# Kernel tuning notes

Hardware: AMD Instinct MI355X
Metric: run time of the kernel (lower is better)

## Reference

```python
import jax, jax.numpy as jnp
import numpy as np
import math

B, S, DIN, DQ, DV = 8, 2048, 1024, 1024, 1024


def setup_inputs() -> dict:
    key = jax.random.key(0)
    ks = jax.random.split(key, 9)
    c_q = math.sqrt(6.0 / (DIN + DQ))
    c_v = math.sqrt(6.0 / (DIN + DV))
    query = jax.random.normal(ks[0], (B, S, DIN), dtype=jnp.float32)
    key_t = jax.random.normal(ks[1], (B, S, DIN), dtype=jnp.float32)
    value = jax.random.normal(ks[2], (B, S, DIN), dtype=jnp.float32)
    # Linear weights stored as [in, out] for x @ W; uniform init per module
    Wq = jax.random.uniform(ks[3], (DIN, DQ), jnp.float32, -c_q, c_q)
    Wk = jax.random.uniform(ks[4], (DIN, DQ), jnp.float32, -c_q, c_q)
    Wv = jax.random.uniform(ks[5], (DIN, DV), jnp.float32, -c_v, c_v)
    bq = jax.random.uniform(ks[6], (DQ,), jnp.float32, -c_q, c_q)
    bk = jax.random.uniform(ks[7], (DQ,), jnp.float32, -c_q, c_q)
    bv = jax.random.uniform(ks[8], (DV,), jnp.float32, -c_v, c_v)
    # causal mask: True where attention is disallowed (masked_fill semantics)
    mask = jnp.broadcast_to(jnp.triu(jnp.ones((S, S), dtype=bool), k=1), (B, S, S))
    return {"query": query, "key": key_t, "value": value,
            "Wq": Wq, "bq": bq, "Wk": Wk, "bk": bk, "Wv": Wv, "bv": bv,
            "mask": mask}


def reference(query, key, value, Wq, bq, Wk, bk, Wv, bv, mask):
    q = query @ Wq + bq                       # [B,S,DQ]
    k = key @ Wk + bk                         # [B,S,DQ]
    v = value @ Wv + bv                       # [B,S,DV]
    scores = jnp.einsum('bsd,btd->bst', q, k) / math.sqrt(DQ)  # [B,S,S]
    scores = jnp.where(mask, jnp.float32(-1e9), scores)
    weights = jax.nn.softmax(scores, axis=2)
    y = jnp.einsum('bst,btd->bsd', weights, v)  # [B,S,DV]
    return y
```

## Files before the change

kernel.cpp:

```cpp
#include <hip/hip_runtime.h>


typedef unsigned short u16;
typedef unsigned int   u32;
typedef float f32x4 __attribute__((ext_vector_type(4)));
typedef short s16x8 __attribute__((ext_vector_type(8)));

__device__ __forceinline__ u16 f2bf(float x) {
  u32 u = __builtin_bit_cast(u32, x);
  u += 0x7fffu + ((u >> 16) & 1u);
  return (u16)(u >> 16);
}
__device__ __forceinline__ float bf2f(u16 h) {
  u32 u = (u32)h << 16;
  return __builtin_bit_cast(float, u);
}

__device__ __forceinline__ void gld_lds16(const u16* g, u16* l) {
  __builtin_amdgcn_global_load_lds((const __attribute__((address_space(1))) void*)g,
                                   (__attribute__((address_space(3))) void*)l,
                                   16, 0, 0);
}

__global__ __launch_bounds__(256) void cvt_bf16_3(const float* __restrict__ i0,
                                                  const float* __restrict__ i1,
                                                  const float* __restrict__ i2,
                                                  u16* __restrict__ out, long X) {
  const float* in = blockIdx.y == 0 ? i0 : (blockIdx.y == 1 ? i1 : i2);
  long i = (long)blockIdx.x * 256 + threadIdx.x;
  float4 v = ((const float4*)in)[i];
  ushort4 o;
  o.x = f2bf(v.x); o.y = f2bf(v.y); o.z = f2bf(v.z); o.w = f2bf(v.w);
  ((ushort4*)(out + blockIdx.y * X))[i] = o;
}

__global__ __launch_bounds__(256) void transpose_w3(const float* __restrict__ w0,
                                                    const float* __restrict__ w1,
                                                    const float* __restrict__ w2,
                                                    u16* __restrict__ Wt,
                                                    int K, int N, long WN) {
  __shared__ u16 t[32][33];
  const float* W = blockIdx.z == 0 ? w0 : (blockIdx.z == 1 ? w1 : w2);
  u16* out = Wt + blockIdx.z * WN;
  int n0 = blockIdx.x * 32, k0 = blockIdx.y * 32;
  int tx = threadIdx.x & 31, ty = threadIdx.x >> 5;
  for (int r = ty; r < 32; r += 8)
    t[r][tx] = f2bf(W[(long)(k0 + r) * N + n0 + tx]);
  __syncthreads();
  for (int r = ty; r < 32; r += 8)
    out[(long)(n0 + r) * K + k0 + tx] = t[tx][r];
}

__global__ __launch_bounds__(256) void transpose_v(const u16* __restrict__ v,
                                                   u16* __restrict__ vt,
                                                   int S, int D) {
  __shared__ u16 t[32][33];
  long b = blockIdx.z;
  const u16* vb = v + b * S * D;
  u16* vtb = vt + b * S * D;
  int d0 = blockIdx.x * 32, s0 = blockIdx.y * 32;
  int tx = threadIdx.x & 31, ty = threadIdx.x >> 5;
  for (int r = ty; r < 32; r += 8)
    t[r][tx] = vb[(long)(s0 + r) * D + d0 + tx];
  __syncthreads();
  for (int r = ty; r < 32; r += 8)
    vtb[(long)(d0 + r) * S + s0 + tx] = t[tx][r];
}

__device__ __forceinline__ void gemm_core(const u16* __restrict__ At,
                                          const u16* __restrict__ Bt,
                                          int lda, int ldb, int ktEnd,
                                          f32x4 (&acc)[4][4],
                                          u16* lA, u16* lB) {
  const int tid = threadIdx.x;
  const int lane = tid & 63, half = lane >> 4, l16 = lane & 15;
  const int wave = tid >> 6;
  const int wm = (wave >> 1) * 64, wn = (wave & 1) * 64;

  const int c0 = tid, c1 = tid + 256;
  const int r0 = c0 >> 2, kp0 = (c0 & 3) ^ ((c0 >> 3) & 3);
  const int r1 = c1 >> 2, kp1 = (c1 & 3) ^ ((c1 >> 3) & 3);
  const u16* gA0 = At + (long)r0 * lda + kp0 * 8;
  const u16* gA1 = At + (long)r1 * lda + kp1 * 8;
  const u16* gB0 = Bt + (long)r0 * ldb + kp0 * 8;
  const u16* gB1 = Bt + (long)r1 * ldb + kp1 * 8;
  u16* lA0 = lA + c0 * 8; u16* lA1 = lA + c1 * 8;
  u16* lB0 = lB + c0 * 8; u16* lB1 = lB + c1 * 8;
  const int swz = (half ^ ((l16 >> 1) & 3)) * 8;

  for (int kt = 0; kt < ktEnd; ++kt) {
    const int k0 = kt * 32;
    gld_lds16(gA0 + k0, lA0);
    gld_lds16(gA1 + k0, lA1);
    gld_lds16(gB0 + k0, lB0);
    gld_lds16(gB1 + k0, lB1);
    __syncthreads();
    s16x8 af[4], bfr[4];
#pragma unroll
    for (int mi = 0; mi < 4; ++mi)
      af[mi] = *(const s16x8*)&lA[(wm + mi * 16 + l16) * 32 + swz];
#pragma unroll
    for (int ni = 0; ni < 4; ++ni)
      bfr[ni] = *(const s16x8*)&lB[(wn + ni * 16 + l16) * 32 + swz];
#pragma unroll
    for (int mi = 0; mi < 4; ++mi)
#pragma unroll
      for (int ni = 0; ni < 4; ++ni)
        acc[mi][ni] = __builtin_amdgcn_mfma_f32_16x16x32_bf16(af[mi], bfr[ni], acc[mi][ni], 0, 0, 0);
    __syncthreads();
  }
}

struct ProjPtrs {
  const u16* A[3];
  const u16* B[3];
  u16* C[3];
  const float* bias[3];
};

__global__ __launch_bounds__(256, 2)
void gemm_proj(ProjPtrs p, int lda, int ldb, int ldc, int kTiles) {
  const int f = blockIdx.x;
  const int xcd = f & 7;
  const int g = f >> 3;
  const int bz = g >> 7;
  const int l = g & 127;
  const int bm = (xcd << 4) + (l >> 3);
  const int bn = l & 7;

  __shared__ u16 lA[128 * 32], lB[128 * 32];
  f32x4 acc[4][4];
#pragma unroll
  for (int i = 0; i < 4; ++i)
#pragma unroll
    for (int j = 0; j < 4; ++j) { f32x4 z = {0.f, 0.f, 0.f, 0.f}; acc[i][j] = z; }

  gemm_core(p.A[bz] + (long)bm * 128 * lda, p.B[bz] + (long)bn * 128 * ldb,
            lda, ldb, kTiles, acc, lA, lB);

  const int lane = threadIdx.x & 63, half = lane >> 4, l16 = lane & 15;
  const int wave = threadIdx.x >> 6;
  const int wm = (wave >> 1) * 64, wn = (wave & 1) * 64;
  const int colBase = bn * 128 + wn + l16;
  const int rowBase = bm * 128 + wm + half * 4;
  u16* Cb = p.C[bz];
  const float* bias = p.bias[bz];
#pragma unroll
  for (int mi = 0; mi < 4; ++mi)
#pragma unroll
    for (int ni = 0; ni < 4; ++ni) {
      int col = colBase + ni * 16;
      float bv = bias[col];
#pragma unroll
      for (int r = 0; r < 4; ++r)
        Cb[(long)(rowBase + mi * 16 + r) * ldc + col] = f2bf(acc[mi][ni][r] + bv);
    }
}

__global__ __launch_bounds__(256, 2)
void gemm_scores_exp(const u16* __restrict__ q, const u16* __restrict__ k,
                     u16* __restrict__ E, int ld, long sQK, long sSC,
                     int kTiles, float scale) {
  const int f = blockIdx.x;
  const int bz = f & 7;
  const int t = f >> 3;
  int bm = (int)((sqrtf(8.f * t + 1.f) - 1.f) * 0.5f);
  while ((bm + 1) * (bm + 2) / 2 <= t) ++bm;
  while (bm * (bm + 1) / 2 > t) --bm;
  const int bn = t - bm * (bm + 1) / 2;

  __shared__ u16 lA[128 * 32], lB[128 * 32];
  f32x4 acc[4][4];
#pragma unroll
  for (int i = 0; i < 4; ++i)
#pragma unroll
    for (int j = 0; j < 4; ++j) { f32x4 z = {0.f, 0.f, 0.f, 0.f}; acc[i][j] = z; }

  gemm_core(q + (long)bz * sQK + (long)bm * 128 * ld,
            k + (long)bz * sQK + (long)bn * 128 * ld,
            ld, ld, kTiles, acc, lA, lB);

  const int lane = threadIdx.x & 63, half = lane >> 4, l16 = lane & 15;
  const int wave = threadIdx.x >> 6;
  const int wm = (wave >> 1) * 64, wn = (wave & 1) * 64;
  u16* Eb = E + (long)bz * sSC;
  const int colBase = bn * 128 + wn + l16;
  const int rowBase = bm * 128 + wm + half * 4;
  const bool diag = (bn == bm);
#pragma unroll
  for (int mi = 0; mi < 4; ++mi)
#pragma unroll
    for (int ni = 0; ni < 4; ++ni) {
      int col = colBase + ni * 16;
#pragma unroll
      for (int r = 0; r < 4; ++r) {
        int row = rowBase + mi * 16 + r;
        float e = __expf(acc[mi][ni][r] * scale);
        u16 out = (!diag || col <= row) ? f2bf(e) : (u16)0;
        Eb[(long)row * 2048 + col] = out;
      }
    }
}

__global__ __launch_bounds__(256) void row_inv(const u16* __restrict__ E,
                                               float* __restrict__ inv, int S) {
  const int wave = threadIdx.x >> 6, lane = threadIdx.x & 63;
  const long row = (long)blockIdx.x * 4 + wave;
  const int i = (int)(row & (S - 1));
  const int zend = ((i >> 7) + 1) << 7;
  const u16* erow = E + row * S;
  float s = 0.f;
  for (int c = lane * 4; c < zend; c += 256) {
    ushort4 u = *(const ushort4*)(erow + c);
    s += (bf2f(u.x) + bf2f(u.y)) + (bf2f(u.z) + bf2f(u.w));
  }
  for (int o = 32; o > 0; o >>= 1) s += __shfl_down(s, o);
  if (lane == 0) inv[row] = 1.f / s;
}

__global__ __launch_bounds__(256, 2)
void gemm_pv(const u16* __restrict__ E, const u16* __restrict__ vT,
             const float* __restrict__ inv, float* __restrict__ y,
             int lda, int ldb, int ldc, long sP, long sV, long sY, int S) {
  const int f = blockIdx.x;
  const int bz = f & 7;
  const int g = f >> 3;
  const int bm = 15 - (g >> 3);
  const int bn = g & 7;
  const int ktEnd = (bm + 1) * 4;

  __shared__ u16 lA[128 * 32], lB[128 * 32];
  f32x4 acc[4][4];
#pragma unroll
  for (int i = 0; i < 4; ++i)
#pragma unroll
    for (int j = 0; j < 4; ++j) { f32x4 z = {0.f, 0.f, 0.f, 0.f}; acc[i][j] = z; }

  gemm_core(E + (long)bz * sP + (long)bm * 128 * lda,
            vT + (long)bz * sV + (long)bn * 128 * ldb,
            lda, ldb, ktEnd, acc, lA, lB);

  const int lane = threadIdx.x & 63, half = lane >> 4, l16 = lane & 15;
  const int wave = threadIdx.x >> 6;
  const int wm = (wave >> 1) * 64, wn = (wave & 1) * 64;
  float* Cb = y + (long)bz * sY;
  const float* invb = inv + (long)bz * S;
  const int colBase = bn * 128 + wn + l16;
  const int rowBase = bm * 128 + wm + half * 4;
#pragma unroll
  for (int mi = 0; mi < 4; ++mi) {
    float iv[4];
#pragma unroll
    for (int r = 0; r < 4; ++r) iv[r] = invb[rowBase + mi * 16 + r];
#pragma unroll
    for (int ni = 0; ni < 4; ++ni) {
      int col = colBase + ni * 16;
#pragma unroll
      for (int r = 0; r < 4; ++r)
        Cb[(long)(rowBase + mi * 16 + r) * ldc + col] = acc[mi][ni][r] * iv[r];
    }
  }
}

extern "C" void kernel_launch(void* const* d_in, const int* in_sizes, int n_in,
                              void* d_out, int out_size, void* d_ws, size_t ws_size,
                              hipStream_t stream) {
  const int B = 8, S = 2048, DIN = 1024, DQ = 1024, DV = 1024;
  const long X  = (long)B * S * DIN;
  const long WN = (long)DIN * DQ;

  const float* query = (const float*)d_in[0];
  const float* key   = (const float*)d_in[1];
  const float* value = (const float*)d_in[2];
  const float* Wq = (const float*)d_in[3];
  const float* bq = (const float*)d_in[4];
  const float* Wk = (const float*)d_in[5];
  const float* bk = (const float*)d_in[6];
  const float* Wv = (const float*)d_in[7];
  const float* bv = (const float*)d_in[8];

  u16* w = (u16*)d_ws;
  u16* xq = w;
  u16* WT = w + 3 * X;
  const long R1 = 3 * X + 3 * WN;
  u16* vbuf = w + R1;
  u16* q  = w + R1 + X;
  u16* k  = w + R1 + 2 * X;
  u16* vT = w + R1 + 3 * X;
  u16* E = w;
  float* inv = (float*)(w + 3 * X);

  dim3 blk(256);
  cvt_bf16_3<<<dim3(X / 1024, 3), blk, 0, stream>>>(query, key, value, xq, X);
  transpose_w3<<<dim3(DQ / 32, DIN / 32, 3), blk, 0, stream>>>(Wq, Wk, Wv, WT, DIN, DQ, WN);

  ProjPtrs pp;
  pp.A[0] = xq; pp.A[1] = xq + X; pp.A[2] = xq + 2 * X;
  pp.B[0] = WT; pp.B[1] = WT + WN; pp.B[2] = WT + 2 * WN;
  pp.C[0] = q;  pp.C[1] = k;      pp.C[2] = vbuf;
  pp.bias[0] = bq; pp.bias[1] = bk; pp.bias[2] = bv;
  gemm_proj<<<dim3(3072), blk, 0, stream>>>(pp, DIN, DIN, DQ, DIN / 32);

  transpose_v<<<dim3(DV / 32, S / 32, B), blk, 0, stream>>>(vbuf, vT, S, DV);

  gemm_scores_exp<<<dim3(136 * 8), blk, 0, stream>>>(
      q, k, E, DQ, X / B, (long)S * S, DQ / 32, 0.03125f);

  row_inv<<<dim3(B * S / 4), blk, 0, stream>>>(E, inv, S);

  gemm_pv<<<dim3(1024), blk, 0, stream>>>(
      E, vT, inv, (float*)d_out, S, S, DV, (long)S * S, (long)DV * S,
      (long)S * DV, S);
}
```

Before: 587.2 us.

## Rewrite projection GEMM as 256x256-tile, 512-thread kernel with 4-stage LDS pipeline

The QKV projection GEMM moves from 128x128 tiles with 256 threads and the shared gemm_core to a dedicated 256x256-tile kernel with 8 waves. It uses a 4-deep ring of LDS buffers filled by direct global-to-LDS loads, explicit vmcnt/lgkmcnt waits, split barriers and s_setprio around the MFMA blocks, so loads overlap with compute. The larger tiles cut global and LDS traffic per FLOP. In exchange it needs 128 KB of LDS per block and more registers per wave, which lowers occupancy, and it hardcodes the 1024 dimensions.

Result: faster. 572.5 us (-2.5%).

```diff
diff --git a/kernel.cpp b/kernel.cpp
--- a/kernel.cpp
+++ b/kernel.cpp
@@ -118,42 +118,120 @@
   const float* bias[3];
 };
 
-__global__ __launch_bounds__(256, 2)
-void gemm_proj(ProjPtrs p, int lda, int ldb, int ldc, int kTiles) {
+__global__ __launch_bounds__(512, 2)
+void gemm_proj(ProjPtrs p) {
+  const int H = 32;
   const int f = blockIdx.x;
-  const int xcd = f & 7;
-  const int g = f >> 3;
-  const int bz = g >> 7;
-  const int l = g & 127;
-  const int bm = (xcd << 4) + (l >> 3);
-  const int bn = l & 7;
-
-  __shared__ u16 lA[128 * 32], lB[128 * 32];
-  f32x4 acc[4][4];
-#pragma unroll
-  for (int i = 0; i < 4; ++i)
+  const int wg = (f & 7) * 96 + (f >> 3);
+  const int bz = wg >> 8;
+  const int rr = wg & 255;
+  const int bm = rr >> 2, bn = rr & 3;
+
+  __shared__ u16 lds[65536];
+  u16* lA = lds;
+  u16* lB = lds + 32768;
+
+  const int tid = threadIdx.x;
+  const int lane = tid & 63, l16 = lane & 15, lq = lane >> 4;
+  const int w = tid >> 6;
+  const int wm = (w >> 2) * 128, wn = (w & 3) * 64;
+
+  const u16* At = p.A[bz] + (long)bm * 256 * 1024;
+  const u16* Bt = p.B[bz] + (long)bn * 256 * 1024;
+
+  const int srow = tid >> 2;
+  const int skp  = (tid & 3) ^ ((tid >> 3) & 3);
+  const u16* gA = At + srow * 1024 + skp * 8;
+  const u16* gB = Bt + srow * 1024 + skp * 8;
+  const int o0 = tid * 8, o1 = tid * 8 + 4096;
+
+  const int fsw = (lq ^ ((l16 >> 1) & 3)) << 3;
+  const int aoff = (wm + l16) * 32 + fsw;
+  const int boff = (wn + l16) * 32 + fsw;
+
+  f32x4 acc[8][4];
+#pragma unroll
+  for (int i = 0; i < 8; ++i)
 #pragma unroll
     for (int j = 0; j < 4; ++j) { f32x4 z = {0.f, 0.f, 0.f, 0.f}; acc[i][j] = z; }
 
-  gemm_core(p.A[bz] + (long)bm * 128 * lda, p.B[bz] + (long)bn * 128 * ldb,
-            lda, ldb, kTiles, acc, lA, lB);
-
-  const int lane = threadIdx.x & 63, half = lane >> 4, l16 = lane & 15;
-  const int wave = threadIdx.x >> 6;
-  const int wm = (wave >> 1) * 64, wn = (wave & 1) * 64;
-  const int colBase = bn * 128 + wn + l16;
-  const int rowBase = bm * 128 + wm + half * 4;
+#define STA(h) { u16* s_ = lA + ((h) & 3) * 8192;                 \
+                 gld_lds16(gA + (h) * 32, s_ + o0);               \
+                 gld_lds16(gA + (h) * 32 + 128 * 1024, s_ + o1); }
+#define STB(h) { u16* s_ = lB + ((h) & 3) * 8192;                 \
+                 gld_lds16(gB + (h) * 32, s_ + o0);               \
+                 gld_lds16(gB + (h) * 32 + 128 * 1024, s_ + o1); }
+#define FENCE asm volatile("" ::: "memory")
+
+  STA(0); STB(0); STA(1); STB(1); STA(2); STB(2);
+  asm volatile("s_waitcnt vmcnt(8)" ::: "memory");
+  __builtin_amdgcn_s_barrier();
+  FENCE;
+
+  for (int t = 0; t < H; ++t) {
+    u16* sA = lA + (t & 3) * 8192;
+    u16* sB = lB + (t & 3) * 8192;
+    s16x8 af[4], bfr[4];
+#pragma unroll
+    for (int mi = 0; mi < 4; ++mi)
+      af[mi] = *(const s16x8*)&sA[aoff + mi * 512];
+#pragma unroll
+    for (int ni = 0; ni < 4; ++ni)
+      bfr[ni] = *(const s16x8*)&sB[boff + ni * 512];
+    if (t + 3 < H) STA(t + 3);
+    FENCE;
+    __builtin_amdgcn_s_barrier();
+    asm volatile("s_waitcnt lgkmcnt(0)" ::: "memory");
+    __builtin_amdgcn_s_setprio(1);
+#pragma unroll
+    for (int mi = 0; mi < 4; ++mi)
+#pragma unroll
+      for (int ni = 0; ni < 4; ++ni)
+        acc[mi][ni] = __builtin_amdgcn_mfma_f32_16x16x32_bf16(af[mi], bfr[ni], acc[mi][ni], 0, 0, 0);
+    __builtin_amdgcn_s_setprio(0);
+    FENCE;
+    __builtin_amdgcn_s_barrier();
+    FENCE;
+#pragma unroll
+    for (int mi = 0; mi < 4; ++mi)
+      af[mi] = *(const s16x8*)&sA[aoff + 2048 + mi * 512];
+    if (t + 3 < H) STB(t + 3);
+    FENCE;
+    __builtin_amdgcn_s_barrier();
+    asm volatile("s_waitcnt lgkmcnt(0)" ::: "memory");
+    __builtin_amdgcn_s_setprio(1);
+#pragma unroll
+    for (int mi = 0; mi < 4; ++mi)
+#pragma unroll
+      for (int ni = 0; ni < 4; ++ni)
+        acc[4 + mi][ni] = __builtin_amdgcn_mfma_f32_16x16x32_bf16(af[mi], bfr[ni], acc[4 + mi][ni], 0, 0, 0);
+    __builtin_amdgcn_s_setprio(0);
+    if (t < H - 3)       { asm volatile("s_waitcnt vmcnt(8)" ::: "memory"); }
+    else if (t == H - 3) { asm volatile("s_waitcnt vmcnt(4)" ::: "memory"); }
+    else if (t == H - 2) { asm volatile("s_waitcnt vmcnt(0)" ::: "memory"); }
+    FENCE;
+    __builtin_amdgcn_s_barrier();
+    FENCE;
+  }
+#undef STA
+#undef STB
+#undef FENCE
+
   u16* Cb = p.C[bz];
   const float* bias = p.bias[bz];
-#pragma unroll
-  for (int mi = 0; mi < 4; ++mi)
+  const int colBase = bn * 256 + wn + l16;
+  const long rowBase = (long)bm * 256 + wm + lq * 4;
+  float bvv[4];
+#pragma unroll
+  for (int ni = 0; ni < 4; ++ni) bvv[ni] = bias[colBase + ni * 16];
+#pragma unroll
+  for (int mi = 0; mi < 8; ++mi)
 #pragma unroll
     for (int ni = 0; ni < 4; ++ni) {
-      int col = colBase + ni * 16;
-      float bv = bias[col];
+      const int col = colBase + ni * 16;
 #pragma unroll
       for (int r = 0; r < 4; ++r)
-        Cb[(long)(rowBase + mi * 16 + r) * ldc + col] = f2bf(acc[mi][ni][r] + bv);
+        Cb[(rowBase + mi * 16 + r) * 1024 + col] = f2bf(acc[mi][ni][r] + bvv[ni]);
     }
 }
 
@@ -299,7 +377,7 @@
   pp.B[0] = WT; pp.B[1] = WT + WN; pp.B[2] = WT + 2 * WN;
   pp.C[0] = q;  pp.C[1] = k;      pp.C[2] = vbuf;
   pp.bias[0] = bq; pp.bias[1] = bk; pp.bias[2] = bv;
-  gemm_proj<<<dim3(3072), blk, 0, stream>>>(pp, DIN, DIN, DQ, DIN / 32);
+  gemm_proj<<<dim3(768), dim3(512), 0, stream>>>(pp);
 
   transpose_v<<<dim3(DV / 32, S / 32, B), blk, 0, stream>>>(vbuf, vT, S, DV);
 
```

## Rewrite projection GEMM with 256x256 tiles, 512 threads, and pipelined LDS double buffering

Applied to the files above, without the earlier changes.

The QKV projection GEMM moves from 128x128 tiles on 256-thread blocks to 256x256 tiles on 512-thread blocks. It uses a double-buffered 128KB LDS with direct global-to-LDS loads, a k-tile of 64, and a hand-scheduled phase loop with explicit waitcnt, barriers and setprio around the MFMA groups. The aim is higher arithmetic intensity per tile and overlap of global loads with MFMA work. The block-to-XCD mapping is also changed and the bias loads are hoisted out of the store loop. Dimensions are hardcoded, and the large LDS footprint and accumulator set may limit occupancy.

Result: faster. 571.1 us (-2.7%).

```diff
diff --git a/kernel.cpp b/kernel.cpp
--- a/kernel.cpp
+++ b/kernel.cpp
@@ -118,42 +118,122 @@
   const float* bias[3];
 };
 
-__global__ __launch_bounds__(256, 2)
-void gemm_proj(ProjPtrs p, int lda, int ldb, int ldc, int kTiles) {
+__global__ __launch_bounds__(512, 2)
+void gemm_proj(ProjPtrs p) {
+  const int NT = 16;
+  const int NIT = 8;
   const int f = blockIdx.x;
-  const int xcd = f & 7;
-  const int g = f >> 3;
-  const int bz = g >> 7;
-  const int l = g & 127;
-  const int bm = (xcd << 4) + (l >> 3);
-  const int bn = l & 7;
-
-  __shared__ u16 lA[128 * 32], lB[128 * 32];
-  f32x4 acc[4][4];
-#pragma unroll
-  for (int i = 0; i < 4; ++i)
+  const int wg = (f & 7) * 96 + (f >> 3);
+  const int bz = wg >> 8;
+  const int rr = wg & 255;
+  const int bm = rr >> 2, bn = rr & 3;
+
+  __shared__ u16 lds[65536];
+  u16* lA = lds;
+  u16* lB = lds + 32768;
+
+  const int tid = threadIdx.x;
+  const int lane = tid & 63, l16 = lane & 15, lq = lane >> 4;
+  const int w = tid >> 6;
+
+  const u16* At = p.A[bz] + (long)bm * 256 * 1024;
+  const u16* Bt = p.B[bz] + (long)bn * 256 * 1024;
+
+  const int sr = tid >> 3;
+  const int sc = (tid & 7) ^ (sr & 7);
+  const long sO0 = (long)sr * 1024 + sc * 8;
+  const int swz0 = ((lq) ^ (l16 & 7)) * 8;
+  const int swz1 = ((4 + lq) ^ (l16 & 7)) * 8;
+  const int aBase = (w >> 2) * 8192 + l16 * 64;
+  const int bBase = ((w & 3) >> 1) * 8192 + (((w & 3) & 1) * 64 + l16) * 64;
+
+  f32x4 acc[8][4];
+#pragma unroll
+  for (int i = 0; i < 8; ++i)
 #pragma unroll
     for (int j = 0; j < 4; ++j) { f32x4 z = {0.f, 0.f, 0.f, 0.f}; acc[i][j] = z; }
 
-  gemm_core(p.A[bz] + (long)bm * 128 * lda, p.B[bz] + (long)bn * 128 * ldb,
-            lda, ldb, kTiles, acc, lA, lB);
-
-  const int lane = threadIdx.x & 63, half = lane >> 4, l16 = lane & 15;
-  const int wave = threadIdx.x >> 6;
-  const int wm = (wave >> 1) * 64, wn = (wave & 1) * 64;
-  const int colBase = bn * 128 + wn + l16;
-  const int rowBase = bm * 128 + wm + half * 4;
+  s16x8 af[4], bf0[4], bf1[4];
+
+#define STG(ldsM, gM, buf, h, kt) {                               \
+    u16* d_ = (ldsM) + (buf) * 16384 + (h) * 8192 + tid * 8;      \
+    const u16* s_ = (gM) + (long)(h) * 131072 + (long)(kt) * 64;  \
+    gld_lds16(s_ + sO0, d_);                                      \
+    gld_lds16(s_ + sO0 + 65536, d_ + 4096); }
+#define RD_AF(BUF, MH, SWZ)                                       \
+    _Pragma("unroll") for (int mi = 0; mi < 4; ++mi)              \
+      af[mi] = *(const s16x8*)&lA[(BUF) * 16384 + aBase + ((MH) * 4 + mi) * 1024 + (SWZ)];
+#define RD_BF(BUF, BF, SWZ)                                       \
+    _Pragma("unroll") for (int ni = 0; ni < 4; ++ni)              \
+      BF[ni] = *(const s16x8*)&lB[(BUF) * 16384 + bBase + ni * 1024 + (SWZ)];
+#define COMPUTE(MH, BF)                                           \
+    __builtin_amdgcn_sched_barrier(0);                            \
+    __builtin_amdgcn_s_barrier();                                 \
+    asm volatile("s_waitcnt lgkmcnt(0)" ::: "memory");            \
+    __builtin_amdgcn_sched_barrier(0);                            \
+    __builtin_amdgcn_s_setprio(1);                                \
+    _Pragma("unroll") for (int mi = 0; mi < 4; ++mi)              \
+      _Pragma("unroll") for (int ni = 0; ni < 4; ++ni)            \
+        acc[(MH) * 4 + mi][ni] = __builtin_amdgcn_mfma_f32_16x16x32_bf16(af[mi], BF[ni], acc[(MH) * 4 + mi][ni], 0, 0, 0); \
+    __builtin_amdgcn_s_setprio(0);
+#define ENDPH __builtin_amdgcn_s_barrier();
+#define VM2 asm volatile("s_waitcnt vmcnt(2)" ::: "memory");
+#define VM0 asm volatile("s_waitcnt vmcnt(0)" ::: "memory");
+
+  STG(lB, Bt, 0, 0, 0); STG(lB, Bt, 0, 1, 0);
+  STG(lA, At, 0, 0, 0); STG(lA, At, 0, 1, 0);
+  STG(lB, Bt, 1, 0, 1);
+  VM2;
+  __builtin_amdgcn_s_barrier();
+
+  for (int i = 0; i < NIT; ++i) {
+    const int ta = 2 * i, tb = 2 * i + 1;
+    const bool st = (i < NIT - 1);
+    RD_AF(0, 0, swz0); RD_BF(0, bf0, swz0); STG(lB, Bt, 1, 1, tb);
+    COMPUTE(0, bf0); ENDPH;
+    RD_AF(0, 1, swz0); STG(lA, At, 1, 0, tb);
+    COMPUTE(1, bf0); ENDPH;
+    RD_AF(0, 0, swz1); RD_BF(0, bf1, swz1); STG(lA, At, 1, 1, tb);
+    COMPUTE(0, bf1); ENDPH;
+    RD_AF(0, 1, swz1); if (st) STG(lB, Bt, 0, 0, ta + 2);
+    COMPUTE(1, bf1);
+    if (st) { VM2 } else { VM0 }
+    ENDPH;
+    RD_AF(1, 0, swz0); RD_BF(1, bf0, swz0); if (st) STG(lB, Bt, 0, 1, ta + 2);
+    COMPUTE(0, bf0); ENDPH;
+    RD_AF(1, 1, swz0); if (st) STG(lA, At, 0, 0, ta + 2);
+    COMPUTE(1, bf0); ENDPH;
+    RD_AF(1, 0, swz1); RD_BF(1, bf1, swz1); if (st) STG(lA, At, 0, 1, ta + 2);
+    COMPUTE(0, bf1); ENDPH;
+    RD_AF(1, 1, swz1); if (st) STG(lB, Bt, 1, 0, tb + 2);
+    COMPUTE(1, bf1);
+    if (st) { VM2 }
+    ENDPH;
+  }
+#undef STG
+#undef RD_AF
+#undef RD_BF
+#undef COMPUTE
+#undef ENDPH
+#undef VM2
+#undef VM0
+
+  const int wm = (w >> 2) * 128, wn = (w & 3) * 64;
   u16* Cb = p.C[bz];
   const float* bias = p.bias[bz];
-#pragma unroll
-  for (int mi = 0; mi < 4; ++mi)
+  const int colBase = bn * 256 + wn + l16;
+  const long rowBase = (long)bm * 256 + wm + lq * 4;
+  float bvv[4];
+#pragma unroll
+  for (int ni = 0; ni < 4; ++ni) bvv[ni] = bias[colBase + ni * 16];
+#pragma unroll
+  for (int mi = 0; mi < 8; ++mi)
 #pragma unroll
     for (int ni = 0; ni < 4; ++ni) {
-      int col = colBase + ni * 16;
-      float bv = bias[col];
+      const int col = colBase + ni * 16;
 #pragma unroll
       for (int r = 0; r < 4; ++r)
-        Cb[(long)(rowBase + mi * 16 + r) * ldc + col] = f2bf(acc[mi][ni][r] + bv);
+        Cb[(rowBase + mi * 16 + r) * 1024 + col] = f2bf(acc[mi][ni][r] + bvv[ni]);
     }
 }
 
@@ -299,7 +379,7 @@
   pp.B[0] = WT; pp.B[1] = WT + WN; pp.B[2] = WT + 2 * WN;
   pp.C[0] = q;  pp.C[1] = k;      pp.C[2] = vbuf;
   pp.bias[0] = bq; pp.bias[1] = bk; pp.bias[2] = bv;
-  gemm_proj<<<dim3(3072), blk, 0, stream>>>(pp, DIN, DIN, DQ, DIN / 32);
+  gemm_proj<<<dim3(768), dim3(512), 0, stream>>>(pp);
 
   transpose_v<<<dim3(DV / 32, S / 32, B), blk, 0, stream>>>(vbuf, vT, S, DV);
 
```
